# Performance work log

Measured on AMD Instinct MI355X. Metric: run time of the kernel, lower is better.

## Reference

```python
import jax, jax.numpy as jnp
import numpy as np

B, N, C = 4, 1024, 512
H = 8
HD = C // H
SCALE = HD ** (-0.5)


def setup_inputs() -> dict:
    key = jax.random.key(0)
    ks = jax.random.split(key, 12)
    s = 0.02
    return {
        "x": jax.random.normal(ks[0], (B, N, C), dtype=jnp.float32),
        "y": jax.random.normal(ks[1], (B, N, C), dtype=jnp.float32),
        "Wqkv1": jax.random.normal(ks[2], (4 * C, C), dtype=jnp.float32) * s,
        "Wqkv2": jax.random.normal(ks[3], (4 * C, C), dtype=jnp.float32) * s,
        "W1": jax.random.normal(ks[4], (C, C), dtype=jnp.float32) * s,
        "b1": jnp.zeros((C,), dtype=jnp.float32),
        "W2": jax.random.normal(ks[5], (C, C), dtype=jnp.float32) * s,
        "b2": jnp.zeros((C,), dtype=jnp.float32),
        "W3": jax.random.normal(ks[6], (C, C), dtype=jnp.float32) * s,
        "b3": jnp.zeros((C,), dtype=jnp.float32),
        "W4": jax.random.normal(ks[7], (C, C), dtype=jnp.float32) * s,
        "b4": jnp.zeros((C,), dtype=jnp.float32),
    }


def _l2norm(t, eps=1e-12):
    # matches F.normalize(dim=-1)
    n = jnp.sqrt(jnp.sum(t * t, axis=-1, keepdims=True))
    return t / jnp.maximum(n, eps)


def _ortho_loss(q, qt):
    # q, qt: [B, H, N, HD]
    qn = _l2norm(q)
    qtn = _l2norm(qt)
    prod = jnp.einsum("bhnd,bhmd->bhnm", qn, qtn)  # [B,H,N,N]
    eye = jnp.eye(N, dtype=prod.dtype)
    off = prod * (1.0 - eye)
    # fro-norm squared of off-diagonal, divided by B*N*N (as in source)
    return jnp.sum(off * off) / (B * N * N)


def _qkv(inp, W):
    # inp: [B,N,C], W: [4C, C] -> [4, B, H, N, HD]
    t = (inp @ W.T).reshape(B, N, 4, H, HD)
    return jnp.transpose(t, (2, 0, 3, 1, 4))


def _attn(q, k, v):
    # q,k,v: [B,H,N,HD] -> [B,N,C]
    scores = jnp.einsum("bhnd,bhmd->bhnm", q, k) * SCALE
    a = jax.nn.softmax(scores, axis=-1)
    o = jnp.einsum("bhnm,bhmd->bhnd", a, v)
    return jnp.transpose(o, (0, 2, 1, 3)).reshape(B, N, C)


def reference(x, y, Wqkv1, Wqkv2, W1, b1, W2, b2, W3, b3, W4, b4):
    qkv1 = _qkv(x, Wqkv1)
    qkv2 = _qkv(y, Wqkv2)
    qx, kx, vx, qtx = qkv1[0], qkv1[1], qkv1[2], qkv1[3]
    qy, ky, vy, qty = qkv2[0], qkv2[1], qkv2[2], qkv2[3]

    lorthx = _ortho_loss(qx, qtx)
    lorthy = _ortho_loss(qy, qty)

    yc = _attn(qx, ky, vy)  # attncy @ vy
    xc = _attn(qy, kx, vx)  # attncx @ vx
    xt = _attn(qtx, kx, vx)
    yt = _attn(qty, ky, vy)

    xc = xc @ W1.T + b1
    yc = yc @ W2.T + b2
    xt = xt @ W3.T + b3
    yt = yt @ W4.T + b4

    # pairwise cosine distance between normalized xc, yc
    xcn = _l2norm(xc)
    ycn = _l2norm(yc)
    cos = jnp.sum(xcn * ycn, axis=-1)
    lc = jnp.mean(1.0 - cos)

    return (xc, yc, xt, yt, lorthx, lorthy, lc)
```

## Files before the change

### kernel.cpp

```cpp
#include <hip/hip_runtime.h>

typedef unsigned short u16;
typedef __attribute__((ext_vector_type(4))) unsigned short u16x4;
typedef __attribute__((ext_vector_type(8))) unsigned short u16x8;
typedef __attribute__((ext_vector_type(4))) float          f32x4;
typedef __attribute__((ext_vector_type(8))) __bf16         bf16x8;

#define MFMA16(a,b,c) __builtin_amdgcn_mfma_f32_16x16x32_bf16((a),(b),(c),0,0,0)
#define SCALE 0.125f
#define SCALE_LOG2E 0.18033688011112042f

__device__ __forceinline__ u16 f2b(float f){
  unsigned u = __builtin_bit_cast(unsigned, f);
  u = (u + 0x7fffu + ((u >> 16) & 1u)) >> 16;
  return (u16)u;
}
__device__ __forceinline__ u16 f2b_trunc(float f){
  return (u16)(__builtin_bit_cast(unsigned, f) >> 16);
}
__device__ __forceinline__ float b2f(u16 v){
  unsigned u = ((unsigned)v) << 16;
  return __builtin_bit_cast(float, u);
}
__device__ __forceinline__ void async16(const u16* g, u16* l){
  __builtin_amdgcn_global_load_lds(
      (const __attribute__((address_space(1))) unsigned*)g,
      (__attribute__((address_space(3))) unsigned*)l, 16, 0, 0);
}
__device__ __forceinline__ int swz(int row, int chunk, int off){
  return row*64 + (((chunk ^ row ^ (row >> 3)) & 7) << 3) + off;
}

__global__ void cast_all_k(const float* __restrict__ x, const float* __restrict__ y,
                           const float* __restrict__ wq1, const float* __restrict__ wq2,
                           const float* __restrict__ w1, const float* __restrict__ w2,
                           const float* __restrict__ w3, const float* __restrict__ w4,
                           u16* __restrict__ dst){
  int i = blockIdx.x * 256 + threadIdx.x;
  const float* s; int base; float sc = 1.f;
  if      (i < 524288)  { s = x;   base = 0;       }
  else if (i < 1048576) { s = y;   base = 524288;  }
  else if (i < 1310720) { s = wq1; base = 1048576;
    int iw = i - base; if (iw < 65536 || iw >= 196608) sc = SCALE_LOG2E; }
  else if (i < 1572864) { s = wq2; base = 1310720;
    int iw = i - base; if (iw < 65536 || iw >= 196608) sc = SCALE_LOG2E; }
  else if (i < 1638400) { s = w1;  base = 1572864; }
  else if (i < 1703936) { s = w2;  base = 1638400; }
  else if (i < 1769472) { s = w3;  base = 1703936; }
  else                  { s = w4;  base = 1769472; }
  float4 v = ((const float4*)s)[i - base];
  u16x4 o; o[0]=f2b(v.x*sc); o[1]=f2b(v.y*sc); o[2]=f2b(v.z*sc); o[3]=f2b(v.w*sc);
  ((u16x4*)dst)[i] = o;
}

__global__ __launch_bounds__(256, 2) void qkv_mega_k(
    const u16* __restrict__ xb, const u16* __restrict__ Wq,
    u16* __restrict__ qkv, u16* __restrict__ vT)
{
  const int i = blockIdx.x;
  const u16 *A, *B; u16* C; int ldc, m0, n0;
  if (i < 512) {
    int z = i >> 8, t = i & 255;
    m0 = (t & 31)*128; n0 = (t >> 5)*128;
    A = xb + (size_t)z*2097152; B = Wq + (size_t)z*1048576;
    C = qkv + (size_t)z*8388608; ldc = 2048;
  } else if (i < 768) {
    int z = (i-512) >> 7, t = (i-512) & 127;
    m0 = (t & 31)*128; n0 = (t >> 5)*128;
    A = xb + (size_t)z*2097152; B = Wq + (size_t)z*1048576 + (size_t)1536*512;
    C = qkv + (size_t)z*8388608 + 1536; ldc = 2048;
  } else {
    int z = (i-768) >> 7, t = (i-768) & 127;
    m0 = (t & 3)*128; n0 = (t >> 2)*128;
    A = Wq + (size_t)z*1048576 + (size_t)1024*512; B = xb + (size_t)z*2097152;
    C = vT + (size_t)z*2097152; ldc = 4096;
  }

  __shared__ u16 As[128*32];
  __shared__ u16 Bs[128*32];
  const int tid  = threadIdx.x;
  const int w    = tid >> 6, lane = tid & 63;
  const int quad = lane >> 4, l16 = lane & 15;
  const int wr   = w >> 1, wc = w & 1;

  f32x4 acc[4][4] = {};
  const int rowa = lane >> 2;
  const int ko   = (lane & 3) * 8;

  for (int k0 = 0; k0 < 512; k0 += 32) {
    __syncthreads();
#pragma unroll
    for (int r = 0; r < 2; ++r) {
      int rb = (r*4 + w) * 16;
      async16(A + (size_t)(m0 + rb + rowa)*512 + k0 + ko, As + (r*4 + w)*512);
      async16(B + (size_t)(n0 + rb + rowa)*512 + k0 + ko, Bs + (r*4 + w)*512);
    }
    __syncthreads();
    bf16x8 af[4], bfr[4];
#pragma unroll
    for (int ii = 0; ii < 4; ++ii)
      af[ii] = *(const bf16x8*)&As[(wr*64 + ii*16 + l16)*32 + quad*8];
#pragma unroll
    for (int j = 0; j < 4; ++j)
      bfr[j] = *(const bf16x8*)&Bs[(wc*64 + j*16 + l16)*32 + quad*8];
#pragma unroll
    for (int ii = 0; ii < 4; ++ii)
#pragma unroll
      for (int j = 0; j < 4; ++j)
        acc[ii][j] = MFMA16(af[ii], bfr[j], acc[ii][j]);
  }
#pragma unroll
  for (int j = 0; j < 4; ++j) {
    int col = n0 + wc*64 + j*16 + l16;
#pragma unroll
    for (int ii = 0; ii < 4; ++ii)
#pragma unroll
      for (int reg = 0; reg < 4; ++reg) {
        int row = m0 + wr*64 + ii*16 + quad*4 + reg;
        C[(size_t)row*ldc + col] = f2b(acc[ii][j][reg]);
      }
  }
}

__global__ __launch_bounds__(256, 2) void gemm_fin_k(
    const u16* __restrict__ A0, size_t aStr, const u16* __restrict__ B0, size_t bStr,
    const float* __restrict__ bias0, const float* __restrict__ bias1,
    const float* __restrict__ bias2, const float* __restrict__ bias3,
    float* __restrict__ C0, size_t cStr)
{
  const int z = blockIdx.z;
  const u16* A = A0 + (size_t)z * aStr;
  const u16* Bm = B0 + (size_t)z * bStr;
  float* Cb = C0 + (size_t)z * cStr;
  const float* bias = (z==0) ? bias0 : (z==1) ? bias1 : (z==2) ? bias2 : bias3;

  __shared__ u16 As[128*32];
  __shared__ u16 Bs[128*32];
  const int tid  = threadIdx.x;
  const int w    = tid >> 6, lane = tid & 63;
  const int quad = lane >> 4, l16 = lane & 15;
  const int wr   = w >> 1, wc = w & 1;
  const int m0 = blockIdx.x * 128, n0 = blockIdx.y * 128;

  f32x4 acc[4][4] = {};
  const int rowa = lane >> 2;
  const int ko   = (lane & 3) * 8;

  for (int k0 = 0; k0 < 512; k0 += 32) {
    __syncthreads();
#pragma unroll
    for (int r = 0; r < 2; ++r) {
      int rb = (r*4 + w) * 16;
      async16(A  + (size_t)(m0 + rb + rowa)*512 + k0 + ko, As + (r*4 + w)*512);
      async16(Bm + (size_t)(n0 + rb + rowa)*512 + k0 + ko, Bs + (r*4 + w)*512);
    }
    __syncthreads();
    bf16x8 af[4], bfr[4];
#pragma unroll
    for (int ii = 0; ii < 4; ++ii)
      af[ii] = *(const bf16x8*)&As[(wr*64 + ii*16 + l16)*32 + quad*8];
#pragma unroll
    for (int j = 0; j < 4; ++j)
      bfr[j] = *(const bf16x8*)&Bs[(wc*64 + j*16 + l16)*32 + quad*8];
#pragma unroll
    for (int ii = 0; ii < 4; ++ii)
#pragma unroll
      for (int j = 0; j < 4; ++j)
        acc[ii][j] = MFMA16(af[ii], bfr[j], acc[ii][j]);
  }
#pragma unroll
  for (int j = 0; j < 4; ++j) {
    int col = n0 + wc*64 + j*16 + l16;
    float bv = bias[col];
#pragma unroll
    for (int ii = 0; ii < 4; ++ii)
#pragma unroll
      for (int reg = 0; reg < 4; ++reg) {
        int row = m0 + wr*64 + ii*16 + quad*4 + reg;
        Cb[(size_t)row*512 + col] = acc[ii][j][reg] + bv;
      }
  }
}

__global__ __launch_bounds__(256, 2) void attn_k(
    const u16* __restrict__ qkv1, const u16* __restrict__ qkv2,
    const u16* __restrict__ vT1, const u16* __restrict__ vT2,
    u16* __restrict__ ao)
{
  const int qt = blockIdx.x, bh = blockIdx.y, p = blockIdx.z;
  const int b = bh >> 3, h = bh & 7;
  const u16* kvsrc = p ? qkv2 : qkv1;
  const u16* vsrc  = p ? vT2 : vT1;
  const u16* qsrcA = p ? qkv1 : qkv2;  const int qoffA = h*64;
  const u16* qsrcB = p ? qkv2 : qkv1;  const int qoffB = 1536 + h*64;
  const int koff = 512 + h*64;
  const size_t tb = (size_t)b * 1024;

  __shared__ u16 Ks[2][4096];
  __shared__ u16 Vt[2][4096];
  __shared__ u16 Ps[4][2][1024];

  const int tid = threadIdx.x, w = tid >> 6, lane = tid & 63;
  const int quad = lane >> 4, l16 = lane & 15;
  const int srow = tid >> 3, sch = tid & 7;

  u16x8 onesu;
#pragma unroll
  for (int ii = 0; ii < 8; ++ii) onesu[ii] = 0x3f80;
  const bf16x8 ONES = __builtin_bit_cast(bf16x8, onesu);

  bf16x8 qb[2][2][2];
#pragma unroll
  for (int s2 = 0; s2 < 2; ++s2) {
    size_t row = tb + qt*128 + w*32 + s2*16 + l16;
    const u16* qrA = qsrcA + row*2048 + qoffA;
    const u16* qrB = qsrcB + row*2048 + qoffB;
    qb[0][s2][0] = *(const bf16x8*)(qrA + quad*8);
    qb[0][s2][1] = *(const bf16x8*)(qrA + 32 + quad*8);
    qb[1][s2][0] = *(const bf16x8*)(qrB + quad*8);
    qb[1][s2][1] = *(const bf16x8*)(qrB + 32 + quad*8);
  }

  f32x4 oacc[2][2][4] = {};
  f32x4 lacc[2][2] = {};

  u16x8 kreg[2], vreg[2];
  auto loadTile = [&](int t){
#pragma unroll
    for (int r = 0; r < 2; ++r) {
      kreg[r] = *(const u16x8*)(kvsrc + (tb + t*64 + r*32 + srow)*2048 + koff + sch*8);
      vreg[r] = *(const u16x8*)(vsrc + (size_t)(h*64 + r*32 + srow)*4096 + tb + t*64 + sch*8);
    }
  };
  auto storeTile = [&](int buf){
#pragma unroll
    for (int r = 0; r < 2; ++r) {
      *(u16x8*)&Ks[buf][swz(r*32 + srow, sch, 0)] = kreg[r];
      *(u16x8*)&Vt[buf][swz(r*32 + srow, sch, 0)] = vreg[r];
    }
  };

  loadTile(0);
  storeTile(0);
  loadTile(1);

  for (int kt = 0; kt < 16; ++kt) {
    const int cur = kt & 1;
    __syncthreads();
    if (kt < 15) storeTile(cur ^ 1);
    if (kt < 14) loadTile(kt + 2);

    bf16x8 ka[4][2], vb[4][2];
#pragma unroll
    for (int j = 0; j < 4; ++j) {
      ka[j][0] = *(const bf16x8*)&Ks[cur][swz(j*16 + l16, quad, 0)];
      ka[j][1] = *(const bf16x8*)&Ks[cur][swz(j*16 + l16, quad + 4, 0)];
      vb[j][0] = *(const bf16x8*)&Vt[cur][swz(j*16 + l16, quad, 0)];
      vb[j][1] = *(const bf16x8*)&Vt[cur][swz(j*16 + l16, quad + 4, 0)];
    }

    bf16x8 paP0, paP1;
#pragma unroll
    for (int idx = 0; idx < 4; ++idx) {
      const int o = idx >> 1, s2 = idx & 1;
      u16* wP = Ps[w][idx & 1];
      f32x4 t[4];
      __builtin_amdgcn_s_setprio(1);
#pragma unroll
      for (int j = 0; j < 4; ++j) {
        f32x4 z = {};
        z    = MFMA16(ka[j][0], qb[o][s2][0], z);
        t[j] = MFMA16(ka[j][1], qb[o][s2][1], z);
      }
      __builtin_amdgcn_s_setprio(0);
      if (idx > 0) {
        const u16* rP = Ps[w][(idx - 1) & 1];
        paP0 = *(const bf16x8*)&rP[swz(l16, quad, 0)];
        paP1 = *(const bf16x8*)&rP[swz(l16, quad + 4, 0)];
      }
#pragma unroll
      for (int j = 0; j < 4; ++j) {
        u16x4 pk;
#pragma unroll
        for (int reg = 0; reg < 4; ++reg)
          pk[reg] = f2b_trunc(__builtin_amdgcn_exp2f(t[j][reg]));
        *(u16x4*)&wP[swz(l16, j*2 + (quad >> 1), (quad & 1)*4)] = pk;
      }
      if (idx > 0) {
        const int po = (idx - 1) >> 1, ps2 = (idx - 1) & 1;
        __builtin_amdgcn_s_setprio(1);
#pragma unroll
        for (int j = 0; j < 4; ++j) {
          oacc[po][ps2][j] = MFMA16(paP0, vb[j][0], oacc[po][ps2][j]);
          oacc[po][ps2][j] = MFMA16(paP1, vb[j][1], oacc[po][ps2][j]);
        }
        lacc[po][ps2] = MFMA16(paP0, ONES, lacc[po][ps2]);
        lacc[po][ps2] = MFMA16(paP1, ONES, lacc[po][ps2]);
        __builtin_amdgcn_s_setprio(0);
      }
    }
    {
      const u16* rP = Ps[w][1];
      bf16x8 pa0 = *(const bf16x8*)&rP[swz(l16, quad, 0)];
      bf16x8 pa1 = *(const bf16x8*)&rP[swz(l16, quad + 4, 0)];
      __builtin_amdgcn_s_setprio(1);
#pragma unroll
      for (int j = 0; j < 4; ++j) {
        oacc[1][1][j] = MFMA16(pa0, vb[j][0], oacc[1][1][j]);
        oacc[1][1][j] = MFMA16(pa1, vb[j][1], oacc[1][1][j]);
      }
      lacc[1][1] = MFMA16(pa0, ONES, lacc[1][1]);
      lacc[1][1] = MFMA16(pa1, ONES, lacc[1][1]);
      __builtin_amdgcn_s_setprio(0);
    }
  }

#pragma unroll
  for (int o = 0; o < 2; ++o) {
    int a = p + o*2;
    u16* aop = ao + (size_t)a*(4096*512) + (tb + qt*128)*512 + h*64;
#pragma unroll
    for (int s2 = 0; s2 < 2; ++s2) {
#pragma unroll
      for (int reg = 0; reg < 4; ++reg) {
        float linv = 1.f / lacc[o][s2][reg];
        int row = w*32 + s2*16 + quad*4 + reg;
#pragma unroll
        for (int j = 0; j < 4; ++j)
          aop[(size_t)row*512 + j*16 + l16] = f2b(oacc[o][s2][j][reg] * linv);
      }
    }
  }
}

__global__ __launch_bounds__(256, 2) void orthoA_k(
    const u16* __restrict__ qkv1, const u16* __restrict__ qkv2,
    float* __restrict__ Gbuf, float* __restrict__ accum)
{
  const int bh = blockIdx.x, which = blockIdx.y, tg = blockIdx.z;
  const u16* src = which ? qkv2 : qkv1;
  const int b = bh >> 3, h = bh & 7;
  const size_t tb = (size_t)b * 1024;

  __shared__ u16 QnT[4096], QtnT[4096];
  const int tid = threadIdx.x, w = tid >> 6, lane = tid & 63;
  const int quad = lane >> 4, l16 = lane & 15;

  f32x4 gq[4] = {}, gqt[4] = {};
  float diag = 0.f;

  for (int tt = 0; tt < 2; ++tt) {
    int t = tg*2 + tt;
    __syncthreads();
    if (tid < 128) {
      int tok = tid & 63, mat = tid >> 6;
      const u16* pp = src + (tb + t*64 + tok)*2048 + (mat ? 1536 : 0) + h*64;
      u16x8 rowv[8];
#pragma unroll
      for (int i = 0; i < 8; ++i) rowv[i] = *(const u16x8*)(pp + i*8);
      float ss = 0.f;
#pragma unroll
      for (int i = 0; i < 8; ++i)
#pragma unroll
        for (int jj = 0; jj < 8; ++jj) { float f = b2f(rowv[i][jj]); ss += f*f; }
      float inv = 1.f / fmaxf(sqrtf(ss), 1e-12f);
      u16* dst = mat ? QtnT : QnT;
#pragma unroll
      for (int i = 0; i < 8; ++i)
#pragma unroll
        for (int jj = 0; jj < 8; ++jj)
          dst[swz(i*8 + jj, tok >> 3, tok & 7)] = f2b(b2f(rowv[i][jj]) * inv);
      if (mat == 0) {
        const u16* p2 = src + (tb + t*64 + tok)*2048 + 1536 + h*64;
        float ss2 = 0.f, dot = 0.f;
#pragma unroll
        for (int i = 0; i < 8; ++i) {
          u16x8 r2 = *(const u16x8*)(p2 + i*8);
#pragma unroll
          for (int jj = 0; jj < 8; ++jj) {
            float fq = b2f(rowv[i][jj]), ft = b2f(r2[jj]);
            ss2 += ft*ft; dot += fq*ft;
          }
        }
        float inv2 = 1.f / fmaxf(sqrtf(ss2), 1e-12f);
        float dn = dot * inv * inv2;
        diag += dn * dn;
      }
    }
    __syncthreads();
    bf16x8 a0 = *(const bf16x8*)&QnT [swz(w*16 + l16, quad, 0)];
    bf16x8 a1 = *(const bf16x8*)&QnT [swz(w*16 + l16, quad + 4, 0)];
    bf16x8 t0 = *(const bf16x8*)&QtnT[swz(w*16 + l16, quad, 0)];
    bf16x8 t1 = *(const bf16x8*)&QtnT[swz(w*16 + l16, quad + 4, 0)];
#pragma unroll
    for (int j = 0; j < 4; ++j) {
      bf16x8 b0 = *(const bf16x8*)&QnT [swz(j*16 + l16, quad, 0)];
      bf16x8 b1 = *(const bf16x8*)&QnT [swz(j*16 + l16, quad + 4, 0)];
      gq[j]  = MFMA16(a0, b0, gq[j]);
      gq[j]  = MFMA16(a1, b1, gq[j]);
      bf16x8 c0 = *(const bf16x8*)&QtnT[swz(j*16 + l16, quad, 0)];
      bf16x8 c1 = *(const bf16x8*)&QtnT[swz(j*16 + l16, quad + 4, 0)];
      gqt[j] = MFMA16(t0, c0, gqt[j]);
      gqt[j] = MFMA16(t1, c1, gqt[j]);
    }
  }
  float* Gq = Gbuf + (size_t)((which*32 + bh)*2) * 4096;
  float* Gt = Gq + 4096;
#pragma unroll
  for (int j = 0; j < 4; ++j)
#pragma unroll
    for (int reg = 0; reg < 4; ++reg) {
      int row = w*16 + quad*4 + reg, col = j*16 + l16;
      atomicAdd(&Gq[row*64 + col], gq[j][reg]);
      atomicAdd(&Gt[row*64 + col], gqt[j][reg]);
    }
  if (tid < 64) atomicAdd(&accum[which], -diag);
}

__global__ __launch_bounds__(256, 2) void red_k(
    const float* __restrict__ Gbuf, const float* __restrict__ dout,
    float* __restrict__ accum)
{
  const int tid = threadIdx.x;
  if (blockIdx.x < 64) {
    const int w = tid >> 6, lane = tid & 63;
    const int wid = blockIdx.x * 4 + w;
    float acc = 0.f;
    for (int rr = 0; rr < 16; ++rr) {
      int row = wid*16 + rr;
      const float4* xr = (const float4*)(dout + (size_t)row*512 + lane*8);
      const float4* yr = (const float4*)(dout + 2097152 + (size_t)row*512 + lane*8);
      float4 x0 = xr[0], x1 = xr[1], y0 = yr[0], y1 = yr[1];
      float dxy = x0.x*y0.x + x0.y*y0.y + x0.z*y0.z + x0.w*y0.w
                + x1.x*y1.x + x1.y*y1.y + x1.z*y1.z + x1.w*y1.w;
      float sx  = x0.x*x0.x + x0.y*x0.y + x0.z*x0.z + x0.w*x0.w
                + x1.x*x1.x + x1.y*x1.y + x1.z*x1.z + x1.w*x1.w;
      float sy  = y0.x*y0.x + y0.y*y0.y + y0.z*y0.z + y0.w*y0.w
                + y1.x*y1.x + y1.y*y1.y + y1.z*y1.z + y1.w*y1.w;
#pragma unroll
      for (int off = 32; off > 0; off >>= 1) {
        dxy += __shfl_xor(dxy, off);
        sx  += __shfl_xor(sx,  off);
        sy  += __shfl_xor(sy,  off);
      }
      if (lane == 0) {
        float cosv = dxy / (fmaxf(sqrtf(sx), 1e-12f) * fmaxf(sqrtf(sy), 1e-12f));
        acc += 1.f - cosv;
      }
    }
    if (lane == 0) atomicAdd(&accum[2], acc);
  } else {
    const int i = blockIdx.x - 64;
    const int bh = i & 31, which = i >> 5;
    const float* Gq = Gbuf + (size_t)((which*32 + bh)*2) * 4096;
    const float* Gt = Gq + 4096;
    float acc = 0.f;
    for (int idx = tid*4; idx < 4096; idx += 1024) {
      float4 g  = *(const float4*)(Gq + idx);
      float4 gt = *(const float4*)(Gt + idx);
      acc += g.x*gt.x + g.y*gt.y + g.z*gt.z + g.w*gt.w;
    }
    __shared__ float red[256];
    red[tid] = acc; __syncthreads();
    for (int s2 = 128; s2 > 0; s2 >>= 1) {
      if (tid < s2) red[tid] += red[tid + s2];
      __syncthreads();
    }
    if (tid == 0) atomicAdd(&accum[which], red[0]);
  }
}

__global__ void fin_k(const float* __restrict__ accum, float* __restrict__ outs){
  if (threadIdx.x == 0) {
    outs[0] = accum[0] * (1.f/4194304.f);
    outs[1] = accum[1] * (1.f/4194304.f);
    outs[2] = accum[2] * (1.f/4096.f);
  }
}

extern "C" void kernel_launch(void* const* d_in, const int* in_sizes, int n_in,
                              void* d_out, int out_size, void* d_ws, size_t ws_size,
                              hipStream_t stream)
{
  (void)in_sizes; (void)n_in; (void)out_size; (void)ws_size;
  const float* x     = (const float*)d_in[0];
  const float* y     = (const float*)d_in[1];
  const float* Wqkv1 = (const float*)d_in[2];
  const float* Wqkv2 = (const float*)d_in[3];
  const float* W1 = (const float*)d_in[4];
  const float* b1 = (const float*)d_in[5];
  const float* W2 = (const float*)d_in[6];
  const float* b2 = (const float*)d_in[7];
  const float* W3 = (const float*)d_in[8];
  const float* b3 = (const float*)d_in[9];
  const float* W4 = (const float*)d_in[10];
  const float* b4 = (const float*)d_in[11];

  u16* ws   = (u16*)d_ws;
  u16* xb   = ws;
  u16* Wq1b = ws + (size_t)4194304;
  u16* W1b  = ws + (size_t)6291456;
  u16* qkv1 = ws + (size_t)7340032;
  u16* qkv2 = qkv1 + (size_t)8388608;
  u16* aob  = qkv2 + (size_t)8388608;
  float* accum = (float*)(aob + (size_t)8388608);
  float* Gbuf  = accum + 16;
  u16* vT1 = (u16*)d_out;
  u16* vT2 = vT1 + (size_t)2097152;

  hipMemsetAsync(accum, 0, 16, stream);
  hipMemsetAsync(Gbuf, 0, 2097152, stream);

  cast_all_k<<<dim3(7168), dim3(256), 0, stream>>>(x, y, Wqkv1, Wqkv2, W1, W2, W3, W4, xb);

  qkv_mega_k<<<dim3(1024), dim3(256), 0, stream>>>(xb, Wq1b, qkv1, vT1);

  attn_k<<<dim3(8,32,2), 256, 0, stream>>>(qkv1, qkv2, vT1, vT2, aob);

  orthoA_k<<<dim3(32,2,8), 256, 0, stream>>>(qkv1, qkv2, Gbuf, accum);

  float* outb = (float*)d_out;
  gemm_fin_k<<<dim3(32,4,4), 256, 0, stream>>>(
      aob, 2097152, W1b, 262144, b1, b2, b3, b4, outb, 2097152);

  red_k<<<dim3(128), 256, 0, stream>>>(Gbuf, outb, accum);
  fin_k<<<dim3(1), dim3(64), 0, stream>>>(accum, outb + 8388608);
}
```

Measured before the change: 229.4 us.

## Double-buffer GEMM LDS tiles and remap blocks for XCD-local L2 reuse

Both bf16 GEMM kernels now use two LDS buffers per operand, so the async load of the next K slice is issued while the MFMAs run on the current one. This removes one barrier per iteration and the load-then-compute serialization. The qkv and attention grids are also remapped so that blocks sharing the same data land on the same XCD, which should improve L2 hit rates. The cost is doubled LDS per GEMM block, which could lower occupancy.

Result: no change. 232.0 us (+1.2%).

```diff
diff --git a/kernel.cpp b/kernel.cpp
--- a/kernel.cpp
+++ b/kernel.cpp
@@ -57,7 +57,7 @@
     const u16* __restrict__ xb, const u16* __restrict__ Wq,
     u16* __restrict__ qkv, u16* __restrict__ vT)
 {
-  const int i = blockIdx.x;
+  const int i = (blockIdx.x & 7) * 128 + (blockIdx.x >> 3);
   const u16 *A, *B; u16* C; int ldc, m0, n0;
   if (i < 512) {
     int z = i >> 8, t = i & 255;
@@ -76,38 +76,44 @@
     C = vT + (size_t)z*2097152; ldc = 4096;
   }
 
-  __shared__ u16 As[128*32];
-  __shared__ u16 Bs[128*32];
+  __shared__ u16 As[2][4096];
+  __shared__ u16 Bs[2][4096];
   const int tid  = threadIdx.x;
   const int w    = tid >> 6, lane = tid & 63;
   const int quad = lane >> 4, l16 = lane & 15;
   const int wr   = w >> 1, wc = w & 1;
-
-  f32x4 acc[4][4] = {};
   const int rowa = lane >> 2;
   const int ko   = (lane & 3) * 8;
 
-  for (int k0 = 0; k0 < 512; k0 += 32) {
-    __syncthreads();
+  auto stage = [&](int buf, int k0){
 #pragma unroll
     for (int r = 0; r < 2; ++r) {
       int rb = (r*4 + w) * 16;
-      async16(A + (size_t)(m0 + rb + rowa)*512 + k0 + ko, As + (r*4 + w)*512);
-      async16(B + (size_t)(n0 + rb + rowa)*512 + k0 + ko, Bs + (r*4 + w)*512);
-    }
-    __syncthreads();
+      async16(A + (size_t)(m0 + rb + rowa)*512 + k0 + ko, As[buf] + (r*4 + w)*512);
+      async16(B + (size_t)(n0 + rb + rowa)*512 + k0 + ko, Bs[buf] + (r*4 + w)*512);
+    }
+  };
+
+  f32x4 acc[4][4] = {};
+  stage(0, 0);
+  __syncthreads();
+
+  for (int k0 = 0; k0 < 512; k0 += 32) {
+    const int buf = (k0 >> 5) & 1;
+    if (k0 < 480) stage(buf ^ 1, k0 + 32);
     bf16x8 af[4], bfr[4];
 #pragma unroll
     for (int ii = 0; ii < 4; ++ii)
-      af[ii] = *(const bf16x8*)&As[(wr*64 + ii*16 + l16)*32 + quad*8];
+      af[ii] = *(const bf16x8*)&As[buf][(wr*64 + ii*16 + l16)*32 + quad*8];
 #pragma unroll
     for (int j = 0; j < 4; ++j)
-      bfr[j] = *(const bf16x8*)&Bs[(wc*64 + j*16 + l16)*32 + quad*8];
+      bfr[j] = *(const bf16x8*)&Bs[buf][(wc*64 + j*16 + l16)*32 + quad*8];
 #pragma unroll
     for (int ii = 0; ii < 4; ++ii)
 #pragma unroll
       for (int j = 0; j < 4; ++j)
         acc[ii][j] = MFMA16(af[ii], bfr[j], acc[ii][j]);
+    __syncthreads();
   }
 #pragma unroll
   for (int j = 0; j < 4; ++j) {
@@ -134,39 +140,45 @@
   float* Cb = C0 + (size_t)z * cStr;
   const float* bias = (z==0) ? bias0 : (z==1) ? bias1 : (z==2) ? bias2 : bias3;
 
-  __shared__ u16 As[128*32];
-  __shared__ u16 Bs[128*32];
+  __shared__ u16 As[2][4096];
+  __shared__ u16 Bs[2][4096];
   const int tid  = threadIdx.x;
   const int w    = tid >> 6, lane = tid & 63;
   const int quad = lane >> 4, l16 = lane & 15;
   const int wr   = w >> 1, wc = w & 1;
   const int m0 = blockIdx.x * 128, n0 = blockIdx.y * 128;
-
-  f32x4 acc[4][4] = {};
   const int rowa = lane >> 2;
   const int ko   = (lane & 3) * 8;
 
-  for (int k0 = 0; k0 < 512; k0 += 32) {
-    __syncthreads();
+  auto stage = [&](int buf, int k0){
 #pragma unroll
     for (int r = 0; r < 2; ++r) {
       int rb = (r*4 + w) * 16;
-      async16(A  + (size_t)(m0 + rb + rowa)*512 + k0 + ko, As + (r*4 + w)*512);
-      async16(Bm + (size_t)(n0 + rb + rowa)*512 + k0 + ko, Bs + (r*4 + w)*512);
-    }
-    __syncthreads();
+      async16(A  + (size_t)(m0 + rb + rowa)*512 + k0 + ko, As[buf] + (r*4 + w)*512);
+      async16(Bm + (size_t)(n0 + rb + rowa)*512 + k0 + ko, Bs[buf] + (r*4 + w)*512);
+    }
+  };
+
+  f32x4 acc[4][4] = {};
+  stage(0, 0);
+  __syncthreads();
+
+  for (int k0 = 0; k0 < 512; k0 += 32) {
+    const int buf = (k0 >> 5) & 1;
+    if (k0 < 480) stage(buf ^ 1, k0 + 32);
     bf16x8 af[4], bfr[4];
 #pragma unroll
     for (int ii = 0; ii < 4; ++ii)
-      af[ii] = *(const bf16x8*)&As[(wr*64 + ii*16 + l16)*32 + quad*8];
+      af[ii] = *(const bf16x8*)&As[buf][(wr*64 + ii*16 + l16)*32 + quad*8];
 #pragma unroll
     for (int j = 0; j < 4; ++j)
-      bfr[j] = *(const bf16x8*)&Bs[(wc*64 + j*16 + l16)*32 + quad*8];
+      bfr[j] = *(const bf16x8*)&Bs[buf][(wc*64 + j*16 + l16)*32 + quad*8];
 #pragma unroll
     for (int ii = 0; ii < 4; ++ii)
 #pragma unroll
       for (int j = 0; j < 4; ++j)
         acc[ii][j] = MFMA16(af[ii], bfr[j], acc[ii][j]);
+    __syncthreads();
   }
 #pragma unroll
   for (int j = 0; j < 4; ++j) {
@@ -187,7 +199,11 @@
     const u16* __restrict__ vT1, const u16* __restrict__ vT2,
     u16* __restrict__ ao)
 {
-  const int qt = blockIdx.x, bh = blockIdx.y, p = blockIdx.z;
+  const int lin = blockIdx.x;
+  const int xcd = lin & 7, slot = lin >> 3;
+  const int g   = xcd + 8*(slot >> 3);
+  const int qt  = slot & 7;
+  const int bh  = g >> 1, p = g & 1;
   const int b = bh >> 3, h = bh & 7;
   const u16* kvsrc = p ? qkv2 : qkv1;
   const u16* vsrc  = p ? vT2 : vT1;
@@ -515,7 +531,7 @@
 
   qkv_mega_k<<<dim3(1024), dim3(256), 0, stream>>>(xb, Wq1b, qkv1, vT1);
 
-  attn_k<<<dim3(8,32,2), 256, 0, stream>>>(qkv1, qkv2, vT1, vT2, aob);
+  attn_k<<<dim3(512), 256, 0, stream>>>(qkv1, qkv2, vT1, vT2, aob);
 
   orthoA_k<<<dim3(32,2,8), 256, 0, stream>>>(qkv1, qkv2, Gbuf, accum);
 
```

## Replace Gram atomics with per-tile partial buffers and remap attention blocks per XCD

Applied to the files above, without the earlier changes.

The orthogonality Gram kernel now writes each tile group's partial 64x64 Gram matrices to its own slice of the buffer instead of using float atomicAdd. The reduction kernel sums the 8 partials before taking the dot product, and the Gbuf memset is dropped. The diagonal term is reduced with a warp shuffle so each workgroup issues one atomic instead of 64. The attention grid is flattened to 1D and remapped so the query tiles of the same (batch, head, pair) land on the same XCD for L2 reuse of K and V. In exchange, Gbuf traffic grows fourfold and red_k does more loads.

After: 215.9 us. 1.06x faster.

```diff
diff --git a/kernel.cpp b/kernel.cpp
--- a/kernel.cpp
+++ b/kernel.cpp
@@ -187,7 +187,11 @@
     const u16* __restrict__ vT1, const u16* __restrict__ vT2,
     u16* __restrict__ ao)
 {
-  const int qt = blockIdx.x, bh = blockIdx.y, p = blockIdx.z;
+  const int lin = blockIdx.x;
+  const int xcd = lin & 7, slot = lin >> 3;
+  const int g   = xcd + 8*(slot >> 3);
+  const int qt  = slot & 7;
+  const int bh  = g >> 1, p = g & 1;
   const int b = bh >> 3, h = bh & 7;
   const u16* kvsrc = p ? qkv2 : qkv1;
   const u16* vsrc  = p ? vT2 : vT1;
@@ -404,17 +408,21 @@
       gqt[j] = MFMA16(t1, c1, gqt[j]);
     }
   }
-  float* Gq = Gbuf + (size_t)((which*32 + bh)*2) * 4096;
+  float* Gq = Gbuf + (size_t)((which*32 + bh)*8 + tg) * 8192;
   float* Gt = Gq + 4096;
 #pragma unroll
   for (int j = 0; j < 4; ++j)
 #pragma unroll
     for (int reg = 0; reg < 4; ++reg) {
       int row = w*16 + quad*4 + reg, col = j*16 + l16;
-      atomicAdd(&Gq[row*64 + col], gq[j][reg]);
-      atomicAdd(&Gt[row*64 + col], gqt[j][reg]);
-    }
-  if (tid < 64) atomicAdd(&accum[which], -diag);
+      Gq[row*64 + col] = gq[j][reg];
+      Gt[row*64 + col] = gqt[j][reg];
+    }
+  if (tid < 64) {
+#pragma unroll
+    for (int off = 32; off > 0; off >>= 1) diag += __shfl_xor(diag, off);
+    if (tid == 0) atomicAdd(&accum[which], -diag);
+  }
 }
 
 __global__ __launch_bounds__(256, 2) void red_k(
@@ -452,13 +460,18 @@
   } else {
     const int i = blockIdx.x - 64;
     const int bh = i & 31, which = i >> 5;
-    const float* Gq = Gbuf + (size_t)((which*32 + bh)*2) * 4096;
-    const float* Gt = Gq + 4096;
+    const float* base = Gbuf + (size_t)((which*32 + bh)*8) * 8192;
     float acc = 0.f;
     for (int idx = tid*4; idx < 4096; idx += 1024) {
-      float4 g  = *(const float4*)(Gq + idx);
-      float4 gt = *(const float4*)(Gt + idx);
-      acc += g.x*gt.x + g.y*gt.y + g.z*gt.z + g.w*gt.w;
+      float4 gq = {0.f,0.f,0.f,0.f}, gt = {0.f,0.f,0.f,0.f};
+#pragma unroll
+      for (int t = 0; t < 8; ++t) {
+        float4 a = *(const float4*)(base + (size_t)t*8192 + idx);
+        float4 c = *(const float4*)(base + (size_t)t*8192 + 4096 + idx);
+        gq.x += a.x; gq.y += a.y; gq.z += a.z; gq.w += a.w;
+        gt.x += c.x; gt.y += c.y; gt.z += c.z; gt.w += c.w;
+      }
+      acc += gq.x*gt.x + gq.y*gt.y + gq.z*gt.z + gq.w*gt.w;
     }
     __shared__ float red[256];
     red[tid] = acc; __syncthreads();
@@ -509,13 +522,12 @@
   u16* vT2 = vT1 + (size_t)2097152;
 
   hipMemsetAsync(accum, 0, 16, stream);
-  hipMemsetAsync(Gbuf, 0, 2097152, stream);
 
   cast_all_k<<<dim3(7168), dim3(256), 0, stream>>>(x, y, Wqkv1, Wqkv2, W1, W2, W3, W4, xb);
 
   qkv_mega_k<<<dim3(1024), dim3(256), 0, stream>>>(xb, Wq1b, qkv1, vT1);
 
-  attn_k<<<dim3(8,32,2), 256, 0, stream>>>(qkv1, qkv2, vT1, vT2, aob);
+  attn_k<<<dim3(512), 256, 0, stream>>>(qkv1, qkv2, vT1, vT2, aob);
 
   orthoA_k<<<dim3(32,2,8), 256, 0, stream>>>(qkv1, qkv2, Gbuf, accum);
 
```
